# Kernel optimization log

Measured on AMD Instinct MI355X. Metric: run time of the kernel, lower is better.

Reference implementation:

```python
import jax, jax.numpy as jnp
import numpy as np

EPS = 1e-6

def _layernorm(x, gamma, beta):
    mu = jnp.mean(x, axis=-1, keepdims=True)
    var = jnp.mean(jnp.square(x - mu), axis=-1, keepdims=True)
    return (x - mu) * jax.lax.rsqrt(var + EPS) * gamma + beta


def setup_inputs() -> dict:
    key = jax.random.key(0)
    ks = jax.random.split(key, 8)
    B, N, C, F = 2, 2048, 1024, 4096
    s = 0.02
    return {
        "x": jax.random.normal(ks[0], (B, N, C), jnp.float32),
        "Wq": jax.random.normal(ks[1], (C, C), jnp.float32) * s,
        "Wk": jax.random.normal(ks[2], (C, C), jnp.float32) * s,
        "Wv": jax.random.normal(ks[3], (C, C), jnp.float32) * s,
        "Wp": jax.random.normal(ks[4], (C, C), jnp.float32) * s,
        "bp": jnp.zeros((C,), jnp.float32),
        "W1": jax.random.normal(ks[5], (C, F), jnp.float32) * s,
        "b1": jnp.zeros((F,), jnp.float32),
        "W2": jax.random.normal(ks[6], (F, C), jnp.float32) * s,
        "b2": jnp.zeros((C,), jnp.float32),
        "gamma1": jnp.ones((C,), jnp.float32),
        "beta1": jnp.zeros((C,), jnp.float32),
        "gamma2": jnp.ones((C,), jnp.float32),
        "beta2": jnp.zeros((C,), jnp.float32),
    }


def reference(x, Wq, Wk, Wv, Wp, bp, W1, b1, W2, b2, gamma1, beta1, gamma2, beta2):
    B, N, C = x.shape
    H = 16
    D = C // H
    scale = D ** -0.5

    xn = _layernorm(x, gamma1, beta1)
    # QKV projections (no bias); q pre-scaled by head_dim**-0.5 as in source
    q = (xn @ Wq * scale).reshape(B, N, H, D).transpose(0, 2, 1, 3)  # bhnd
    k = (xn @ Wk).reshape(B, N, H, D).transpose(0, 2, 1, 3)
    v = (xn @ Wv).reshape(B, N, H, D).transpose(0, 2, 1, 3)

    attn = jax.nn.softmax(jnp.einsum("bhnd,bhmd->bhnm", q, k), axis=-1)
    y = jnp.einsum("bhnm,bhmd->bhnd", attn, v)
    y = y.transpose(0, 2, 1, 3).reshape(B, N, C)
    x = x + (y @ Wp + bp)

    xn2 = _layernorm(x, gamma2, beta2)
    h = jax.nn.gelu(xn2 @ W1 + b1, approximate=False)  # keras 'gelu' is exact
    x = x + (h @ W2 + b2)
    return x
```

## Files before the change

### kernel.cpp

```cpp
#include <hip/hip_runtime.h>
#include <math.h>

#define BN  4096
#define SEQ 2048
#define CH  1024
#define FF  4096
#define NH  16
#define HD  64

typedef short bf16x8 __attribute__((ext_vector_type(8)));
typedef float f32x4  __attribute__((ext_vector_type(4)));

#define MFMA16(a,b,c) __builtin_amdgcn_mfma_f32_16x16x32_bf16(a,b,c,0,0,0)

__device__ __forceinline__ unsigned short f2b(float f){
  unsigned u = __float_as_uint(f);
  u += 0x7fffu + ((u>>16)&1u);
  return (unsigned short)(u>>16);
}

__device__ __forceinline__ unsigned pk2(float a, float b){
  return __builtin_amdgcn_perm(__float_as_uint(b), __float_as_uint(a), 0x07060302u);
}

#if __has_builtin(__builtin_amdgcn_exp2f)
__device__ __forceinline__ float fexp2(float x){ return __builtin_amdgcn_exp2f(x); }
#else
__device__ __forceinline__ float fexp2(float x){
  float r; asm("v_exp_f32 %0, %1" : "=v"(r) : "v"(x)); return r;
}
#endif

__device__ __forceinline__ void gl2lds16(const void* g, void* l){
  __builtin_amdgcn_global_load_lds(
      (__attribute__((address_space(1))) void*)g,
      (__attribute__((address_space(3))) void*)l, 16, 0, 0);
}

__global__ __launch_bounds__(256) void transpose_cvt(const float* __restrict__ in,
    unsigned short* __restrict__ out, int R, int S, float scale)
{
  __shared__ float tile[64][65];
  const int tid = threadIdx.x;
  const int tx = tid & 63, ty = tid >> 6;
  const int s0 = blockIdx.x * 64, r0 = blockIdx.y * 64;
  #pragma unroll
  for (int j = 0; j < 16; j++){
    int r = ty + j*4;
    tile[r][tx] = in[(size_t)(r0 + r)*S + s0 + tx];
  }
  __syncthreads();
  #pragma unroll
  for (int j = 0; j < 16; j++){
    int s = ty + j*4;
    out[(size_t)(s0 + s)*R + r0 + tx] = f2b(tile[tx][s] * scale);
  }
}

__global__ __launch_bounds__(256) void ln_kernel(const float* __restrict__ x,
    const float* __restrict__ gamma, const float* __restrict__ beta,
    unsigned short* __restrict__ out)
{
  const int row = blockIdx.x, tid = threadIdx.x;
  const float4 xv = ((const float4*)(x + (size_t)row*CH))[tid];
  float s  = xv.x + xv.y + xv.z + xv.w;
  float ss = xv.x*xv.x + xv.y*xv.y + xv.z*xv.z + xv.w*xv.w;
  #pragma unroll
  for (int off = 1; off < 64; off <<= 1){
    s  += __shfl_xor(s,  off, 64);
    ss += __shfl_xor(ss, off, 64);
  }
  __shared__ float red[8];
  const int w = tid >> 6;
  if ((tid & 63) == 0){ red[w] = s; red[4+w] = ss; }
  __syncthreads();
  s  = red[0]+red[1]+red[2]+red[3];
  ss = red[4]+red[5]+red[6]+red[7];
  const float mu   = s * (1.f/CH);
  const float rstd = rsqrtf(ss*(1.f/CH) - mu*mu + 1e-6f);
  const float4 g = ((const float4*)gamma)[tid];
  const float4 b = ((const float4*)beta )[tid];
  ushort4 o;
  o.x = f2b((xv.x-mu)*rstd*g.x + b.x);
  o.y = f2b((xv.y-mu)*rstd*g.y + b.y);
  o.z = f2b((xv.z-mu)*rstd*g.z + b.z);
  o.w = f2b((xv.w-mu)*rstd*g.w + b.w);
  ((ushort4*)(out + (size_t)row*CH))[tid] = o;
}

template<int BNT,int BIAS,int GELU,int RES,int OMODE,int SPLITK>
__global__ __launch_bounds__(256,2) void gemm_bt(const unsigned short* __restrict__ A,
    const unsigned short* __restrict__ Bt, const float* __restrict__ bias,
    const float* __restrict__ resid, float* __restrict__ outF,
    unsigned short* __restrict__ outB, unsigned short* __restrict__ outK,
    unsigned short* __restrict__ outV, int M, int Nn, int K)
{
  constexpr int MI = (BNT==128) ? 4 : 2;
  constexpr int BCH = (BNT==128) ? 4 : 2;
  __shared__ __align__(16) unsigned short Al[128*64];
  __shared__ __align__(16) unsigned short Bl[BNT*64];
  const int tid = threadIdx.x;
  const int w = tid >> 6, lane = tid & 63;
  const int quad = lane >> 4, l16 = lane & 15;
  const int m0 = blockIdx.y*128, n0 = blockIdx.x*BNT;
  const int wm = (BNT==128) ? (w >> 1)*64 : w*32;
  const int wn = (BNT==128) ? (w & 1)*64 : 0;
  const int srow = lane >> 3, sslot = lane & 7;
  f32x4 acc[MI][4] = {};
  const int kseg = SPLITK > 1 ? K / SPLITK : K;
  const int kBeg = SPLITK > 1 ? blockIdx.z * kseg : 0;
  for (int k0 = kBeg; k0 < kBeg + kseg; k0 += 64){
    __syncthreads();
    #pragma unroll
    for (int i = 0; i < 4; i++){
      const int rb = (w*4 + i)*8;
      const int r = rb + srow;
      const int c = sslot ^ (r & 7);
      gl2lds16(A + (size_t)(m0 + r)*K + k0 + c*8, (char*)Al + rb*128);
    }
    #pragma unroll
    for (int i = 0; i < BCH; i++){
      const int rb = (w*BCH + i)*8;
      const int r = rb + srow;
      const int c = sslot ^ (r & 7);
      gl2lds16(Bt + (size_t)(n0 + r)*K + k0 + c*8, (char*)Bl + rb*128);
    }
    __syncthreads();
    #pragma unroll
    for (int kc = 0; kc < 2; kc++){
      bf16x8 af[MI], bfr[4];
      #pragma unroll
      for (int mi = 0; mi < MI; mi++){
        const int r = wm + mi*16 + l16;
        af[mi] = *(const bf16x8*)(Al + r*64 + (((kc*4 + quad) ^ (r & 7))*8));
      }
      #pragma unroll
      for (int nj = 0; nj < 4; nj++){
        const int r = wn + nj*16 + l16;
        bfr[nj] = *(const bf16x8*)(Bl + r*64 + (((kc*4 + quad) ^ (r & 7))*8));
      }
      #pragma unroll
      for (int mi = 0; mi < MI; mi++)
        #pragma unroll
        for (int nj = 0; nj < 4; nj++)
          acc[mi][nj] = MFMA16(af[mi], bfr[nj], acc[mi][nj]);
    }
  }
  #pragma unroll
  for (int nj = 0; nj < 4; nj++){
    const int col = n0 + wn + nj*16 + l16;
    const float bv = BIAS ? bias[col] : 0.f;
    #pragma unroll
    for (int mi = 0; mi < MI; mi++){
      #pragma unroll
      for (int r = 0; r < 4; r++){
        const int row = m0 + wm + mi*16 + quad*4 + r;
        float v = acc[mi][nj][r];
        if (SPLITK > 1){
          if (blockIdx.z == 0){
            if (BIAS) v += bias[col];
            if (RES)  v += resid[(size_t)row*Nn + col];
          }
          atomicAdd(&outF[(size_t)row*Nn + col], v);
          continue;
        }
        v += bv;
        if (GELU) v = 0.5f*v*(1.f + erff(v*0.70710678118654752f));
        if (RES)  v += resid[(size_t)row*Nn + col];
        if (OMODE == 0) outF[(size_t)row*Nn + col] = v;
        else if (OMODE == 1) outB[(size_t)row*Nn + col] = f2b(v);
        else {
          const int cg = col >> 10, c = col & (CH-1);
          if (cg == 0)      outB[(size_t)row*CH + c] = f2b(v);
          else if (cg == 1) outK[(size_t)row*CH + c] = f2b(v);
          else {
            const int bb = row >> 11, n = row & (SEQ-1);
            const int hh = c >> 6,  d = c & (HD-1);
            const int np = (n & ~63) | (((n & 15) << 2) | ((n >> 4) & 3));
            outV[((size_t)((bb*NH + hh)*HD + d))*SEQ + np] = f2b(v);
          }
        }
      }
    }
  }
}

__global__ __launch_bounds__(256,2) void attn_kernel(const unsigned short* __restrict__ q,
    const unsigned short* __restrict__ k, const unsigned short* __restrict__ vt,
    unsigned short* __restrict__ y)
{
  __shared__ __align__(16) unsigned short Kl[2][64*64];
  __shared__ __align__(16) unsigned short Vl[2][64*64];
  __shared__ __align__(16) unsigned short Pp[4][64*68];
  const int tid = threadIdx.x;
  const int w = tid >> 6, lane = tid & 63;
  const int wq = w & 1, wk = w >> 1;
  const int quad = lane >> 4, l16 = lane & 15;
  const int bh = blockIdx.y;
  const int b = bh >> 4, h = bh & 15;
  const size_t tb  = ((size_t)b*SEQ)*CH + h*HD;
  const size_t vb_ = (size_t)bh*HD*SEQ;
  const int qr0 = blockIdx.x*128 + wq*64;

  bf16x8 qf[4][2];
  #pragma unroll
  for (int mi = 0; mi < 4; mi++)
    #pragma unroll
    for (int kc = 0; kc < 2; kc++)
      qf[mi][kc] = *(const bf16x8*)(q + tb + (size_t)(qr0 + mi*16 + l16)*CH + kc*32 + quad*8);

  float sacc[4][4];
  f32x4 o[4][4] = {};
  #pragma unroll
  for (int mi = 0; mi < 4; mi++)
    #pragma unroll
    for (int r = 0; r < 4; r++) sacc[mi][r] = 0.f;

  for (int t = 0; t < 16; t++){
    const int kv0 = wk*1024 + t*64;
    __syncthreads();
    #pragma unroll
    for (int i = 0; i < 8; i++){
      const int r = i*8 + (lane >> 3);
      const int c = (lane & 7) ^ (r & 7);
      if (wq == 0)
        gl2lds16(k  + tb  + (size_t)(kv0 + r)*CH + c*8, (char*)&Kl[wk][0] + i*1024);
      else
        gl2lds16(vt + vb_ + (size_t)r*SEQ + kv0 + c*8, (char*)&Vl[wk][0] + i*1024);
    }
    __syncthreads();

    f32x4 s[4][4] = {};
    #pragma unroll
    for (int kc = 0; kc < 2; kc++){
      #pragma unroll
      for (int nj = 0; nj < 4; nj++){
        bf16x8 kf = *(const bf16x8*)(&Kl[wk][0] + (nj*16 + l16)*64 + (((kc*4 + quad) ^ (l16 & 7))*8));
        #pragma unroll
        for (int mi = 0; mi < 4; mi++)
          s[mi][nj] = MFMA16(qf[mi][kc], kf, s[mi][nj]);
      }
    }
    #pragma unroll
    for (int mi = 0; mi < 4; mi++){
      #pragma unroll
      for (int r = 0; r < 4; r++){
        const float p0 = fexp2(s[mi][0][r]);
        const float p1 = fexp2(s[mi][1][r]);
        const float p2 = fexp2(s[mi][2][r]);
        const float p3 = fexp2(s[mi][3][r]);
        sacc[mi][r] += (p0 + p1) + (p2 + p3);
        uint2 pk;
        pk.x = pk2(p0, p1);
        pk.y = pk2(p2, p3);
        const int prow = mi*16 + quad*4 + r;
        *(uint2*)(&Pp[w][prow*68 + l16*4]) = pk;
      }
    }
    #pragma unroll
    for (int kc = 0; kc < 2; kc++){
      bf16x8 pa[4];
      #pragma unroll
      for (int mi = 0; mi < 4; mi++)
        pa[mi] = *(const bf16x8*)(&Pp[w][(mi*16 + l16)*68 + kc*32 + quad*8]);
      #pragma unroll
      for (int nd = 0; nd < 4; nd++){
        bf16x8 vf = *(const bf16x8*)(&Vl[wk][0] + (nd*16 + l16)*64 + (((kc*4 + quad) ^ (l16 & 7))*8));
        #pragma unroll
        for (int mi = 0; mi < 4; mi++)
          o[mi][nd] = MFMA16(pa[mi], vf, o[mi][nd]);
      }
    }
  }

  __syncthreads();
  float* ob = wq ? (float*)&Vl[0][0] : (float*)&Kl[0][0];
  float* sb = (float*)&Pp[2 + wq][0];
  if (wk == 1){
    #pragma unroll
    for (int mi = 0; mi < 4; mi++)
      #pragma unroll
      for (int nd = 0; nd < 4; nd++)
        #pragma unroll
        for (int r = 0; r < 4; r++){
          const int idx = (mi*4 + nd)*4 + r;
          ob[lane*64 + ((idx + lane) & 63)] = o[mi][nd][r];
        }
    #pragma unroll
    for (int mi = 0; mi < 4; mi++)
      #pragma unroll
      for (int r = 0; r < 4; r++)
        sb[lane*16 + ((mi*4 + r + lane) & 15)] = sacc[mi][r];
  }
  __syncthreads();
  if (wk == 0){
    #pragma unroll
    for (int mi = 0; mi < 4; mi++)
      #pragma unroll
      for (int nd = 0; nd < 4; nd++)
        #pragma unroll
        for (int r = 0; r < 4; r++){
          const int idx = (mi*4 + nd)*4 + r;
          o[mi][nd][r] += ob[lane*64 + ((idx + lane) & 63)];
        }
    #pragma unroll
    for (int mi = 0; mi < 4; mi++){
      #pragma unroll
      for (int r = 0; r < 4; r++){
        float sum = sacc[mi][r] + sb[lane*16 + ((mi*4 + r + lane) & 15)];
        #pragma unroll
        for (int off = 1; off < 16; off <<= 1) sum += __shfl_xor(sum, off, 64);
        const float inv = 1.f / sum;
        const int qr = qr0 + mi*16 + quad*4 + r;
        #pragma unroll
        for (int nd = 0; nd < 4; nd++)
          y[tb + (size_t)qr*CH + nd*16 + l16] = f2b(o[mi][nd][r]*inv);
      }
    }
  }
}

extern "C" void kernel_launch(void* const* d_in, const int* in_sizes, int n_in,
                              void* d_out, int out_size, void* d_ws, size_t ws_size,
                              hipStream_t stream)
{
  (void)in_sizes; (void)n_in; (void)out_size; (void)ws_size;
  const float* x   = (const float*)d_in[0];
  const float* Wq  = (const float*)d_in[1];
  const float* Wk  = (const float*)d_in[2];
  const float* Wv  = (const float*)d_in[3];
  const float* Wp  = (const float*)d_in[4];
  const float* bp  = (const float*)d_in[5];
  const float* W1  = (const float*)d_in[6];
  const float* b1  = (const float*)d_in[7];
  const float* W2  = (const float*)d_in[8];
  const float* b2  = (const float*)d_in[9];
  const float* g1  = (const float*)d_in[10];
  const float* be1 = (const float*)d_in[11];
  const float* g2  = (const float*)d_in[12];
  const float* be2 = (const float*)d_in[13];
  float* out = (float*)d_out;
  char* ws = (char*)d_ws;
  const size_t MB = 1024*1024;
  unsigned short* wq_t = (unsigned short*)(ws +  0*MB);
  unsigned short* wk_t = (unsigned short*)(ws +  2*MB);
  unsigned short* wv_t = (unsigned short*)(ws +  4*MB);
  unsigned short* wp_t = (unsigned short*)(ws +  6*MB);
  unsigned short* w1_t = (unsigned short*)(ws +  8*MB);
  unsigned short* w2_t = (unsigned short*)(ws + 16*MB);
  unsigned short* xn   = (unsigned short*)(ws + 24*MB);
  unsigned short* qb   = (unsigned short*)(ws + 32*MB);
  unsigned short* kb   = (unsigned short*)(ws + 40*MB);
  unsigned short* vtb  = (unsigned short*)(ws + 48*MB);
  unsigned short* yb   = (unsigned short*)(ws + 56*MB);
  float*          x2   = (float*)         (ws + 64*MB);
  unsigned short* xn2  = (unsigned short*)(ws + 80*MB);
  unsigned short* hb   = (unsigned short*)(ws + 88*MB);

  transpose_cvt<<<dim3(16,16),256,0,stream>>>(Wq, wq_t, CH, CH, 0.18033688011112042f);
  transpose_cvt<<<dim3(16,16),256,0,stream>>>(Wk, wk_t, CH, CH, 1.f);
  transpose_cvt<<<dim3(16,16),256,0,stream>>>(Wv, wv_t, CH, CH, 1.f);
  transpose_cvt<<<dim3(16,16),256,0,stream>>>(Wp, wp_t, CH, CH, 1.f);
  transpose_cvt<<<dim3(64,16),256,0,stream>>>(W1, w1_t, CH, FF, 1.f);
  transpose_cvt<<<dim3(16,64),256,0,stream>>>(W2, w2_t, FF, CH, 1.f);

  ln_kernel<<<BN,256,0,stream>>>(x, g1, be1, xn);
  gemm_bt<128,0,0,0,3,0><<<dim3(24,32),256,0,stream>>>(xn, wq_t, nullptr, nullptr,
      nullptr, qb, kb, vtb, BN, 3072, CH);
  attn_kernel<<<dim3(16,32),256,0,stream>>>(qb, kb, vtb, yb);
  gemm_bt<64,1,0,1,0,0><<<dim3(16,32),256,0,stream>>>(yb, wp_t, bp, x, x2,
      nullptr, nullptr, nullptr, BN, CH, CH);
  ln_kernel<<<BN,256,0,stream>>>(x2, g2, be2, xn2);
  gemm_bt<128,1,1,0,1,0><<<dim3(32,32),256,0,stream>>>(xn2, w1_t, b1, nullptr, nullptr,
      hb, nullptr, nullptr, BN, FF, CH);
  hipMemsetAsync(out, 0, (size_t)BN*CH*sizeof(float), stream);
  gemm_bt<64,1,0,1,0,2><<<dim3(16,32,2),256,0,stream>>>(hb, w2_t, b2, x2, out,
      nullptr, nullptr, nullptr, BN, CH, FF);
}
```

Measured before the change: 360.1 us.

## Double-buffer GEMM LDS tiles and stage bf16 epilogue through LDS for coalescing

The GEMM main loop now keeps two A/B tile buffers in shared memory and prefetches the next K-slice while MFMAs run on the current one, replacing two barriers per step with one. The bf16 output modes now write results into a per-wave LDS scratch area, then store them as 16-byte vectors. This covers the Q/K output and the transposed V layout, so global stores become coalesced instead of scattered 2-byte writes. The cost is twice the LDS footprint, and the epilogue assumes a 64x64 per-wave tile, which may not match every tile configuration that gets launched.

```diff
diff --git a/kernel.cpp b/kernel.cpp
--- a/kernel.cpp
+++ b/kernel.cpp
@@ -95,10 +95,11 @@
     unsigned short* __restrict__ outB, unsigned short* __restrict__ outK,
     unsigned short* __restrict__ outV, int M, int Nn, int K)
 {
-  constexpr int MI = (BNT==128) ? 4 : 2;
+  constexpr int MI  = (BNT==128) ? 4 : 2;
   constexpr int BCH = (BNT==128) ? 4 : 2;
-  __shared__ __align__(16) unsigned short Al[128*64];
-  __shared__ __align__(16) unsigned short Bl[BNT*64];
+  constexpr int ABYTES = 128*64*2;
+  constexpr int BBYTES = BNT*64*2;
+  __shared__ __align__(16) char lds[2*ABYTES + 2*BBYTES];
   const int tid = threadIdx.x;
   const int w = tid >> 6, lane = tid & 63;
   const int quad = lane >> 4, l16 = lane & 15;
@@ -109,35 +110,46 @@
   f32x4 acc[MI][4] = {};
   const int kseg = SPLITK > 1 ? K / SPLITK : K;
   const int kBeg = SPLITK > 1 ? blockIdx.z * kseg : 0;
-  for (int k0 = kBeg; k0 < kBeg + kseg; k0 += 64){
-    __syncthreads();
+  const int nsteps = kseg >> 6;
+
+  auto STAGE = [&](int buf, int k0){
+    char* Ad = lds + buf*ABYTES;
+    char* Bd = lds + 2*ABYTES + buf*BBYTES;
     #pragma unroll
     for (int i = 0; i < 4; i++){
       const int rb = (w*4 + i)*8;
       const int r = rb + srow;
       const int c = sslot ^ (r & 7);
-      gl2lds16(A + (size_t)(m0 + r)*K + k0 + c*8, (char*)Al + rb*128);
+      gl2lds16(A + (size_t)(m0 + r)*K + k0 + c*8, Ad + rb*128);
     }
     #pragma unroll
     for (int i = 0; i < BCH; i++){
       const int rb = (w*BCH + i)*8;
       const int r = rb + srow;
       const int c = sslot ^ (r & 7);
-      gl2lds16(Bt + (size_t)(n0 + r)*K + k0 + c*8, (char*)Bl + rb*128);
-    }
-    __syncthreads();
+      gl2lds16(Bt + (size_t)(n0 + r)*K + k0 + c*8, Bd + rb*128);
+    }
+  };
+
+  STAGE(0, kBeg);
+  __syncthreads();
+  for (int t = 0; t < nsteps; t++){
+    const int cur = t & 1;
+    if (t + 1 < nsteps) STAGE(cur ^ 1, kBeg + (t+1)*64);
+    const unsigned short* Ac = (const unsigned short*)(lds + cur*ABYTES);
+    const unsigned short* Bc = (const unsigned short*)(lds + 2*ABYTES + cur*BBYTES);
     #pragma unroll
     for (int kc = 0; kc < 2; kc++){
       bf16x8 af[MI], bfr[4];
       #pragma unroll
       for (int mi = 0; mi < MI; mi++){
         const int r = wm + mi*16 + l16;
-        af[mi] = *(const bf16x8*)(Al + r*64 + (((kc*4 + quad) ^ (r & 7))*8));
+        af[mi] = *(const bf16x8*)(Ac + r*64 + (((kc*4 + quad) ^ (r & 7))*8));
       }
       #pragma unroll
       for (int nj = 0; nj < 4; nj++){
         const int r = wn + nj*16 + l16;
-        bfr[nj] = *(const bf16x8*)(Bl + r*64 + (((kc*4 + quad) ^ (r & 7))*8));
+        bfr[nj] = *(const bf16x8*)(Bc + r*64 + (((kc*4 + quad) ^ (r & 7))*8));
       }
       #pragma unroll
       for (int mi = 0; mi < MI; mi++)
@@ -145,6 +157,56 @@
         for (int nj = 0; nj < 4; nj++)
           acc[mi][nj] = MFMA16(af[mi], bfr[nj], acc[mi][nj]);
     }
+    __syncthreads();
+  }
+
+  if (OMODE == 1 || OMODE == 3){
+    unsigned short* scr = (unsigned short*)lds + w*(64*64);
+    #pragma unroll
+    for (int nj = 0; nj < 4; nj++){
+      const int col = n0 + wn + nj*16 + l16;
+      const float bv = BIAS ? bias[col] : 0.f;
+      #pragma unroll
+      for (int mi = 0; mi < MI; mi++){
+        #pragma unroll
+        for (int r = 0; r < 4; r++){
+          const int rl = mi*16 + quad*4 + r;
+          float v = acc[mi][nj][r] + bv;
+          if (GELU) v = 0.5f*v*(1.f + erff(v*0.70710678118654752f));
+          if (RES)  v += resid[(size_t)(m0 + wm + rl)*Nn + col];
+          const unsigned short b16 = f2b(v);
+          if (OMODE == 3 && (n0 + wn) >= 2048){
+            const int d = nj*16 + l16;
+            scr[d*64 + (((rl & 15) << 2) | (rl >> 4))] = b16;
+          } else {
+            scr[rl*64 + nj*16 + l16] = b16;
+          }
+        }
+      }
+    }
+    const int row0 = m0 + wm;
+    const int colb = n0 + wn;
+    const int sl = (lane & 7)*8;
+    #pragma unroll
+    for (int j = 0; j < 8; j++){
+      const int rr = j*8 + (lane >> 3);
+      const bf16x8 vv = *(const bf16x8*)(scr + rr*64 + sl);
+      if (OMODE == 1){
+        *(bf16x8*)(outB + (size_t)(row0 + rr)*Nn + colb + sl) = vv;
+      } else {
+        const int cg = colb >> 10;
+        if (cg == 0)
+          *(bf16x8*)(outB + (size_t)(row0 + rr)*CH + (colb & (CH-1)) + sl) = vv;
+        else if (cg == 1)
+          *(bf16x8*)(outK + (size_t)(row0 + rr)*CH + (colb & (CH-1)) + sl) = vv;
+        else {
+          const int bb = row0 >> 11;
+          const int hh = (colb & (CH-1)) >> 6;
+          *(bf16x8*)(outV + ((size_t)((bb*NH + hh)*HD) + rr)*SEQ + (row0 & (SEQ-1)) + sl) = vv;
+        }
+      }
+    }
+    return;
   }
   #pragma unroll
   for (int nj = 0; nj < 4; nj++){
@@ -167,19 +229,7 @@
         v += bv;
         if (GELU) v = 0.5f*v*(1.f + erff(v*0.70710678118654752f));
         if (RES)  v += resid[(size_t)row*Nn + col];
-        if (OMODE == 0) outF[(size_t)row*Nn + col] = v;
-        else if (OMODE == 1) outB[(size_t)row*Nn + col] = f2b(v);
-        else {
-          const int cg = col >> 10, c = col & (CH-1);
-          if (cg == 0)      outB[(size_t)row*CH + c] = f2b(v);
-          else if (cg == 1) outK[(size_t)row*CH + c] = f2b(v);
-          else {
-            const int bb = row >> 11, n = row & (SEQ-1);
-            const int hh = c >> 6,  d = c & (HD-1);
-            const int np = (n & ~63) | (((n & 15) << 2) | ((n >> 4) & 3));
-            outV[((size_t)((bb*NH + hh)*HD + d))*SEQ + np] = f2b(v);
-          }
-        }
+        outF[(size_t)row*Nn + col] = v;
       }
     }
   }
```

New measurement: 370.8 us. 3.0% more time.
